# Performance work log

Hardware: AMD Instinct MI355X
Metric: run time of the kernel (lower is better)

## Reference

```python
import jax, jax.numpy as jnp
import numpy as np

# Instant-NGP style multi-resolution hash grid encoding
L = 16          # n_levels
F = 2           # n_feat_per_entry
D = 3           # spatial dim
T = 2 ** 19     # hashmap entries per level
B = 2 ** 20     # number of query points
BASE_RES, MAX_RES = 16, 512
PRIMES = (1, 2654435761, 805459861)  # NGP spatial hash primes


def setup_inputs() -> dict:
    key = jax.random.key(0)
    k1, k2 = jax.random.split(key)
    xyz = jax.random.uniform(k1, (B, D), dtype=jnp.float32)  # points in [0,1)^3
    offsets = np.arange(L + 1, dtype=np.int32) * T            # len L+1, offsets[-1] = n_total_embed
    n_total = int(offsets[-1])
    embeddings = (jax.random.uniform(k2, (n_total, F), dtype=jnp.float32) * 2.0 - 1.0) * 1e-4
    growth = np.exp(np.log(MAX_RES / BASE_RES) / (L - 1))
    resolutions = np.floor(BASE_RES * growth ** np.arange(L)).astype(np.int32)  # len L
    return {
        "xyz": xyz,
        "embeddings": embeddings,
        "offsets": jnp.asarray(offsets),
        "resolutions": jnp.asarray(resolutions),
        "min_xyz": jnp.zeros((D,), jnp.float32),
        "max_xyz": jnp.ones((D,), jnp.float32),
    }


def _encode(xyz, embeddings, offsets, resolutions, min_xyz, max_xyz):
    Bn, Dn = xyz.shape
    n_grid = 2 ** Dn  # corners of a cell
    # normalize to [0,1]; points outside the box are zeroed (valid mask)
    u = (xyz - min_xyz) / (max_xyz - min_xyz)                      # (B,D)
    valid = jnp.all((u >= 0.0) & (u <= 1.0), axis=-1)              # (B,)
    res = resolutions.astype(xyz.dtype)                            # (L,)
    pos = u[:, None, :] * res[None, :, None]                       # (B,L,D)
    pos0 = jnp.clip(jnp.floor(pos), 0.0, res[None, :, None] - 1.0) # lower cell corner
    frac = pos - pos0                                              # (B,L,D) in [0,1]
    # all 2^D corner offsets, bit d of corner c
    bits = jnp.asarray([[(c >> d) & 1 for d in range(Dn)] for c in range(n_grid)])  # (2^D, D)
    corners = pos0[:, :, None, :].astype(jnp.uint32) + bits[None, None].astype(jnp.uint32)  # (B,L,2^D,D)
    # trilinear weights: prod_d (frac if bit else 1-frac)
    fb = frac[:, :, None, :]
    w = jnp.prod(jnp.where(bits[None, None].astype(bool), fb, 1.0 - fb), axis=-1)  # (B,L,2^D)
    # spatial hash: xor of coord_d * prime_d (uint32 wraparound), mod level table size
    primes = jnp.asarray(PRIMES[:Dn], dtype=jnp.uint32)
    hp = corners * primes                                          # (B,L,2^D,D) uint32
    h = hp[..., 0]
    for d in range(1, Dn):
        h = h ^ hp[..., d]
    sizes = (offsets[1:] - offsets[:-1]).astype(jnp.uint32)        # (L,)
    idx = (h % sizes[None, :, None]).astype(jnp.int32) + offsets[:-1][None, :, None]  # (B,L,2^D)
    gathered = embeddings[idx]                                     # (B,L,2^D,F)
    out = jnp.einsum("blc,blcf->blf", w, gathered)                 # (B,L,F)
    out = out * valid[:, None, None].astype(out.dtype)
    return out.reshape(Bn, -1)                                     # (B, L*F)


def reference(xyz, embeddings, offsets, resolutions, min_xyz, max_xyz):
    return _encode(xyz, embeddings, offsets, resolutions, min_xyz, max_xyz)
```

## Files before the change

### kernel.cpp

```cpp
#include <hip/hip_runtime.h>

#define NLVL 16
#define NDENSE 7
#define BDENSE_CAP 600000

typedef float f32x2 __attribute__((ext_vector_type(2)));
typedef float f32x4 __attribute__((ext_vector_type(4)));
typedef _Float16 f16x2 __attribute__((ext_vector_type(2)));
typedef unsigned u32x2 __attribute__((ext_vector_type(2)));

__device__ __forceinline__ unsigned hash3(unsigned x, unsigned y, unsigned z) {
    return x ^ (y * 2654435761u) ^ (z * 805459861u);
}

__device__ __forceinline__ unsigned bdense_total(const int* __restrict__ resolutions,
                                                 unsigned bdoff[NDENSE]) {
    unsigned acc = 0;
    for (int ll = 0; ll < NDENSE; ++ll) {
        unsigned R = (unsigned)resolutions[ll];
        bdoff[ll] = acc;
        acc += R * R * (R + 1u);
    }
    return acc;
}

__global__ __launch_bounds__(256) void convert_fp16_kernel(
    const float* __restrict__ emb,
    _Float16*    __restrict__ htab,
    int n_entries)
{
    int i = blockIdx.x * 256 + (int)threadIdx.x;
    if (i >= n_entries) return;
    f32x2 v = reinterpret_cast<const f32x2*>(emb)[i];
    f16x2 h;
    h.x = (_Float16)v.x;
    h.y = (_Float16)v.y;
    reinterpret_cast<f16x2*>(htab)[i] = h;
}

__global__ __launch_bounds__(256) void bdensify_kernel(
    const unsigned* __restrict__ htab32,
    const int*      __restrict__ offsets,
    const int*      __restrict__ resolutions,
    unsigned*       __restrict__ bdense)
{
    unsigned bdoff[NDENSE];
    unsigned total = bdense_total(resolutions, bdoff);
    if (total > BDENSE_CAP) total = BDENSE_CAP;
    unsigned tid = blockIdx.x * 256u + threadIdx.x;
    if (tid >= total) return;
    int l = 0;
    while (l < NDENSE - 1 && tid >= bdoff[l + 1]) ++l;
    unsigned idx = tid - bdoff[l];
    unsigned R = (unsigned)resolutions[l];
    unsigned cx = idx % R;
    unsigned t  = idx / R;
    unsigned cy = t % R;
    unsigned z  = t / R;
    unsigned off  = (unsigned)offsets[l];
    unsigned size = (unsigned)offsets[l + 1] - off;
    unsigned mask = size - 1u;
    bool pow2 = (size & mask) == 0u;
    const unsigned* src = htab32 + off;

    unsigned q[4];
    {
        unsigned h = hash3(cx,      cy,      z);
        q[0] = src[pow2 ? (h & mask) : (h % size)];
    }
    {
        unsigned h = hash3(cx + 1u, cy,      z);
        q[1] = src[pow2 ? (h & mask) : (h % size)];
    }
    {
        unsigned h = hash3(cx,      cy + 1u, z);
        q[2] = src[pow2 ? (h & mask) : (h % size)];
    }
    {
        unsigned h = hash3(cx + 1u, cy + 1u, z);
        q[3] = src[pow2 ? (h & mask) : (h % size)];
    }
    __builtin_memcpy(bdense + (size_t)tid * 4u, q, 16);
}

__global__ __launch_bounds__(256) void encode_kernel(
    const float* __restrict__ xyz,
    const float* __restrict__ emb,
    const _Float16* __restrict__ htab,
    const int*   __restrict__ offsets,
    const int*   __restrict__ resolutions,
    const float* __restrict__ min_xyz,
    const float* __restrict__ max_xyz,
    const unsigned* __restrict__ bdense,
    float*       __restrict__ scratch,
    float*       __restrict__ out,
    int B, int use_bdense, int use_scratch, int use_fp16)
{
    const int g = blockIdx.x & 15;
    const int chunk = blockIdx.x >> 4;
    const int l = (g < 8) ? (8 + g) : (((g - 8) + (chunk >> 6)) & 7);
    const int p = chunk * 256 + (int)threadIdx.x;
    if (p >= B) return;

    const float res = (float)resolutions[l];
    const unsigned off  = (unsigned)offsets[l];
    const unsigned size = (unsigned)offsets[l + 1] - off;
    const unsigned mask = size - 1u;
    const bool pow2 = (size & mask) == 0u;
    const float mn0 = min_xyz[0], mn1 = min_xyz[1], mn2 = min_xyz[2];
    const float mx0 = max_xyz[0], mx1 = max_xyz[1], mx2 = max_xyz[2];

    const float x = xyz[p * 3 + 0];
    const float y = xyz[p * 3 + 1];
    const float z = xyz[p * 3 + 2];
    const float ux = (x - mn0) / (mx0 - mn0);
    const float uy = (y - mn1) / (mx1 - mn1);
    const float uz = (z - mn2) / (mx2 - mn2);
    const bool valid = (ux >= 0.0f) & (ux <= 1.0f) &
                       (uy >= 0.0f) & (uy <= 1.0f) &
                       (uz >= 0.0f) & (uz <= 1.0f);

    const float rm1 = res - 1.0f;
    const float px = ux * res, py = uy * res, pz = uz * res;
    const float p0x = fminf(fmaxf(floorf(px), 0.0f), rm1);
    const float p0y = fminf(fmaxf(floorf(py), 0.0f), rm1);
    const float p0z = fminf(fmaxf(floorf(pz), 0.0f), rm1);
    const float fx = px - p0x, fy = py - p0y, fz = pz - p0z;
    const float gx = 1.0f - fx, gy = 1.0f - fy, gz = 1.0f - fz;
    const unsigned cx0 = (unsigned)p0x;
    const unsigned cy0 = (unsigned)p0y;
    const unsigned cz0 = (unsigned)p0z;

    const unsigned P1 = 2654435761u;
    const unsigned P2 = 805459861u;

    float o0 = 0.0f, o1 = 0.0f;

    bool bdense_ok = false;
    unsigned bdoff[NDENSE];
    if (use_bdense && l < NDENSE) {
        unsigned total = bdense_total(resolutions, bdoff);
        bdense_ok = (total <= BDENSE_CAP);
    }

    if (bdense_ok) {
        const unsigned R = (unsigned)resolutions[l];
        const unsigned base = bdoff[l] + (cz0 * R + cy0) * R + cx0;
        unsigned q0[4], q1[4];
        __builtin_memcpy(q0, bdense + (size_t)base * 4u, 16);
        __builtin_memcpy(q1, bdense + (size_t)(base + R * R) * 4u, 16);
        f16x2 e0 = __builtin_bit_cast(f16x2, q0[0]);
        f16x2 e1 = __builtin_bit_cast(f16x2, q0[1]);
        f16x2 e2 = __builtin_bit_cast(f16x2, q0[2]);
        f16x2 e3 = __builtin_bit_cast(f16x2, q0[3]);
        f16x2 e4 = __builtin_bit_cast(f16x2, q1[0]);
        f16x2 e5 = __builtin_bit_cast(f16x2, q1[1]);
        f16x2 e6 = __builtin_bit_cast(f16x2, q1[2]);
        f16x2 e7 = __builtin_bit_cast(f16x2, q1[3]);
        o0 += (gx * gy * gz) * (float)e0.x;  o1 += (gx * gy * gz) * (float)e0.y;
        o0 += (fx * gy * gz) * (float)e1.x;  o1 += (fx * gy * gz) * (float)e1.y;
        o0 += (gx * fy * gz) * (float)e2.x;  o1 += (gx * fy * gz) * (float)e2.y;
        o0 += (fx * fy * gz) * (float)e3.x;  o1 += (fx * fy * gz) * (float)e3.y;
        o0 += (gx * gy * fz) * (float)e4.x;  o1 += (gx * gy * fz) * (float)e4.y;
        o0 += (fx * gy * fz) * (float)e5.x;  o1 += (fx * gy * fz) * (float)e5.y;
        o0 += (gx * fy * fz) * (float)e6.x;  o1 += (gx * fy * fz) * (float)e6.y;
        o0 += (fx * fy * fz) * (float)e7.x;  o1 += (fx * fy * fz) * (float)e7.y;
    } else if (use_fp16 && pow2) {
        const unsigned* lvl32 = reinterpret_cast<const unsigned*>(htab) + off;
        const u32x2*    lvlp  = reinterpret_cast<const u32x2*>(lvl32);
        unsigned m4[4], h0a[4];
        u32x2 pr[4];
#pragma unroll
        for (int pi = 0; pi < 4; ++pi) {
            unsigned by = (unsigned)(pi & 1);
            unsigned bz = (unsigned)(pi >> 1);
            unsigned m = ((cy0 + by) * P1) ^ ((cz0 + bz) * P2);
            unsigned h0 = (cx0 ^ m) & mask;
            m4[pi] = m; h0a[pi] = h0;
            pr[pi] = lvlp[h0 >> 1];
        }
        unsigned e0b[4], e1b[4];
        if ((cx0 & 1u) == 0u) {
#pragma unroll
            for (int pi = 0; pi < 4; ++pi) {
                bool hi = (h0a[pi] & 1u) != 0u;
                e0b[pi] = hi ? pr[pi].y : pr[pi].x;
                e1b[pi] = hi ? pr[pi].x : pr[pi].y;
            }
        } else {
#pragma unroll
            for (int pi = 0; pi < 4; ++pi) {
                unsigned h1 = ((cx0 + 1u) ^ m4[pi]) & mask;
                e1b[pi] = lvl32[h1];
                e0b[pi] = (h0a[pi] & 1u) ? pr[pi].y : pr[pi].x;
            }
        }
#pragma unroll
        for (int pi = 0; pi < 4; ++pi) {
            unsigned by = (unsigned)(pi & 1);
            unsigned bz = (unsigned)(pi >> 1);
            float wy = by ? fy : gy;
            float wz = bz ? fz : gz;
            float wyz = wy * wz;
            f16x2 e0 = __builtin_bit_cast(f16x2, e0b[pi]);
            f16x2 e1 = __builtin_bit_cast(f16x2, e1b[pi]);
            float w0 = gx * wyz;
            float w1 = fx * wyz;
            o0 += w0 * (float)e0.x;  o1 += w0 * (float)e0.y;
            o0 += w1 * (float)e1.x;  o1 += w1 * (float)e1.y;
        }
    } else {
        const f32x2* lvl = reinterpret_cast<const f32x2*>(emb) + off;
#pragma unroll
        for (int c = 0; c < 8; ++c) {
            unsigned bx = (unsigned)(c & 1);
            unsigned by = (unsigned)((c >> 1) & 1);
            unsigned bz = (unsigned)((c >> 2) & 1);
            unsigned h = hash3(cx0 + bx, cy0 + by, cz0 + bz);
            unsigned hm = pow2 ? (h & mask) : (h % size);
            f32x2 e = lvl[hm];
            float w = (bx ? fx : gx) * (by ? fy : gy);
            w = w * (bz ? fz : gz);
            o0 += w * e.x;
            o1 += w * e.y;
        }
    }

    if (!valid) { o0 = 0.0f; o1 = 0.0f; }
    if (use_scratch) {
        f16x2 h; h.x = (_Float16)o0; h.y = (_Float16)o1;
        unsigned hb = __builtin_bit_cast(unsigned, h);
        unsigned* op = reinterpret_cast<unsigned*>(scratch) + (size_t)l * B + p;
        __builtin_nontemporal_store(hb, op);
    } else {
        f32x2 r; r.x = o0; r.y = o1;
        f32x2* op = reinterpret_cast<f32x2*>(out + (size_t)p * (NLVL * 2) + l * 2);
        __builtin_nontemporal_store(r, op);
    }
}

__global__ __launch_bounds__(256) void transpose_kernel(
    const float* __restrict__ scratch,
    float*       __restrict__ out,
    int B)
{
    __shared__ float tile[64][33];
    const int p0 = blockIdx.x * 64;
    const int tid = (int)threadIdx.x;

    const unsigned* src = reinterpret_cast<const unsigned*>(scratch);
#pragma unroll
    for (int k = 0; k < 4; ++k) {
        int it = tid + k * 256;
        int l  = it >> 6;
        int pi = it & 63;
        int p  = p0 + pi;
        unsigned vb = (p < B) ? src[(size_t)l * B + p] : 0u;
        f16x2 v = __builtin_bit_cast(f16x2, vb);
        tile[pi][2 * l]     = (float)v.x;
        tile[pi][2 * l + 1] = (float)v.y;
    }
    __syncthreads();

    const int pl = tid >> 2;
    const int q  = tid & 3;
    const int p  = p0 + pl;
    if (p >= B) return;
    float vals[8];
#pragma unroll
    for (int j = 0; j < 8; ++j) vals[j] = tile[pl][q * 8 + j];
    f32x4 lo, hi;
    lo.x = vals[0]; lo.y = vals[1]; lo.z = vals[2]; lo.w = vals[3];
    hi.x = vals[4]; hi.y = vals[5]; hi.z = vals[6]; hi.w = vals[7];
    f32x4* dst = reinterpret_cast<f32x4*>(out + (size_t)p * 32 + q * 8);
    __builtin_nontemporal_store(lo, dst);
    __builtin_nontemporal_store(hi, dst + 1);
}

extern "C" void kernel_launch(void* const* d_in, const int* in_sizes, int n_in,
                              void* d_out, int out_size, void* d_ws, size_t ws_size,
                              hipStream_t stream) {
    const float* xyz        = (const float*)d_in[0];
    const float* embeddings = (const float*)d_in[1];
    const int*   offsets    = (const int*)d_in[2];
    const int*   resolutions= (const int*)d_in[3];
    const float* min_xyz    = (const float*)d_in[4];
    const float* max_xyz    = (const float*)d_in[5];
    float* out = (float*)d_out;

    int B = in_sizes[0] / 3;
    int n_entries = in_sizes[1] / 2;

    size_t scratch_bytes = (size_t)B * NLVL * 4;
    size_t htab_bytes    = (size_t)n_entries * 4;
    size_t bdense_bytes  = (size_t)BDENSE_CAP * 16;

    int use_scratch = (ws_size >= scratch_bytes) ? 1 : 0;
    size_t htab_off = use_scratch ? scratch_bytes : 0;
    int use_fp16 = (ws_size >= htab_off + htab_bytes) ? 1 : 0;
    size_t bdense_off = htab_off + (use_fp16 ? htab_bytes : 0);
    int use_bdense = (use_fp16 && ws_size >= bdense_off + bdense_bytes) ? 1 : 0;

    float*    scratch = (float*)d_ws;
    _Float16* htab    = (_Float16*)((char*)d_ws + htab_off);
    unsigned* bdense  = (unsigned*)((char*)d_ws + bdense_off);

    if (use_fp16) {
        int cgrid = (n_entries + 255) / 256;
        convert_fp16_kernel<<<cgrid, 256, 0, stream>>>(embeddings, htab, n_entries);
    }
    if (use_bdense) {
        int pgrid = (BDENSE_CAP + 255) / 256;
        bdensify_kernel<<<pgrid, 256, 0, stream>>>(
            (const unsigned*)htab, offsets, resolutions, bdense);
    }
    int nchunks = (B + 255) / 256;
    int grid = nchunks * NLVL;
    encode_kernel<<<grid, 256, 0, stream>>>(
        xyz, embeddings, htab, offsets, resolutions, min_xyz, max_xyz,
        bdense, scratch, out, B, use_bdense, use_scratch, use_fp16);
    if (use_scratch) {
        int tgrid = (B + 63) / 64;
        transpose_kernel<<<tgrid, 256, 0, stream>>>(scratch, out, B);
    }
}
```

Before: 417.1 us.

## Process four points per thread with vectorized xyz loads and scratch stores

Each encode thread now handles four consecutive points. It loads their coordinates with three 16-byte loads, issues all gather loads for the four points before accumulating, and writes the fp16 scratch results as one 16-byte nontemporal store. The aim is more memory-level parallelism per thread and fewer, wider load and store instructions. In exchange, the grid is four times smaller, which lowers occupancy and wave count and raises register pressure. The chunk-based level interleave also changes, since chunk>>6 now spans four times as many points.

Result: faster. 401.3 us (-3.8%).

```diff
diff --git a/kernel.cpp b/kernel.cpp
--- a/kernel.cpp
+++ b/kernel.cpp
@@ -3,11 +3,13 @@
 #define NLVL 16
 #define NDENSE 7
 #define BDENSE_CAP 600000
+#define PPT 4
 
 typedef float f32x2 __attribute__((ext_vector_type(2)));
 typedef float f32x4 __attribute__((ext_vector_type(4)));
 typedef _Float16 f16x2 __attribute__((ext_vector_type(2)));
 typedef unsigned u32x2 __attribute__((ext_vector_type(2)));
+typedef unsigned u32x4 __attribute__((ext_vector_type(4)));
 
 __device__ __forceinline__ unsigned hash3(unsigned x, unsigned y, unsigned z) {
     return x ^ (y * 2654435761u) ^ (z * 805459861u);
@@ -99,8 +101,8 @@
     const int g = blockIdx.x & 15;
     const int chunk = blockIdx.x >> 4;
     const int l = (g < 8) ? (8 + g) : (((g - 8) + (chunk >> 6)) & 7);
-    const int p = chunk * 256 + (int)threadIdx.x;
-    if (p >= B) return;
+    const int p0 = chunk * (256 * PPT) + (int)threadIdx.x * PPT;
+    if (p0 >= B) return;
 
     const float res = (float)resolutions[l];
     const unsigned off  = (unsigned)offsets[l];
@@ -110,31 +112,51 @@
     const float mn0 = min_xyz[0], mn1 = min_xyz[1], mn2 = min_xyz[2];
     const float mx0 = max_xyz[0], mx1 = max_xyz[1], mx2 = max_xyz[2];
 
-    const float x = xyz[p * 3 + 0];
-    const float y = xyz[p * 3 + 1];
-    const float z = xyz[p * 3 + 2];
-    const float ux = (x - mn0) / (mx0 - mn0);
-    const float uy = (y - mn1) / (mx1 - mn1);
-    const float uz = (z - mn2) / (mx2 - mn2);
-    const bool valid = (ux >= 0.0f) & (ux <= 1.0f) &
-                       (uy >= 0.0f) & (uy <= 1.0f) &
-                       (uz >= 0.0f) & (uz <= 1.0f);
-
-    const float rm1 = res - 1.0f;
-    const float px = ux * res, py = uy * res, pz = uz * res;
-    const float p0x = fminf(fmaxf(floorf(px), 0.0f), rm1);
-    const float p0y = fminf(fmaxf(floorf(py), 0.0f), rm1);
-    const float p0z = fminf(fmaxf(floorf(pz), 0.0f), rm1);
-    const float fx = px - p0x, fy = py - p0y, fz = pz - p0z;
-    const float gx = 1.0f - fx, gy = 1.0f - fy, gz = 1.0f - fz;
-    const unsigned cx0 = (unsigned)p0x;
-    const unsigned cy0 = (unsigned)p0y;
-    const unsigned cz0 = (unsigned)p0z;
-
     const unsigned P1 = 2654435761u;
     const unsigned P2 = 805459861u;
 
-    float o0 = 0.0f, o1 = 0.0f;
+    float X[PPT], Y[PPT], Z[PPT];
+    if (p0 + PPT <= B) {
+        f32x4 v0, v1, v2;
+        __builtin_memcpy(&v0, xyz + (size_t)p0 * 3,      16);
+        __builtin_memcpy(&v1, xyz + (size_t)p0 * 3 + 4,  16);
+        __builtin_memcpy(&v2, xyz + (size_t)p0 * 3 + 8,  16);
+        X[0] = v0.x; Y[0] = v0.y; Z[0] = v0.z;
+        X[1] = v0.w; Y[1] = v1.x; Z[1] = v1.y;
+        X[2] = v1.z; Y[2] = v1.w; Z[2] = v2.x;
+        X[3] = v2.y; Y[3] = v2.z; Z[3] = v2.w;
+    } else {
+#pragma unroll
+        for (int i = 0; i < PPT; ++i) {
+            int p = p0 + i; if (p > B - 1) p = B - 1;
+            X[i] = xyz[p * 3 + 0]; Y[i] = xyz[p * 3 + 1]; Z[i] = xyz[p * 3 + 2];
+        }
+    }
+
+    float fxa[PPT], fya[PPT], fza[PPT], qxa[PPT], qya[PPT], qza[PPT];
+    unsigned cxa[PPT], cya[PPT], cza[PPT];
+    bool valid[PPT];
+#pragma unroll
+    for (int i = 0; i < PPT; ++i) {
+        float ux = (X[i] - mn0) / (mx0 - mn0);
+        float uy = (Y[i] - mn1) / (mx1 - mn1);
+        float uz = (Z[i] - mn2) / (mx2 - mn2);
+        valid[i] = (ux >= 0.0f) & (ux <= 1.0f) &
+                   (uy >= 0.0f) & (uy <= 1.0f) &
+                   (uz >= 0.0f) & (uz <= 1.0f);
+        float rm1 = res - 1.0f;
+        float px = ux * res, py = uy * res, pz = uz * res;
+        float p0x = fminf(fmaxf(floorf(px), 0.0f), rm1);
+        float p0y = fminf(fmaxf(floorf(py), 0.0f), rm1);
+        float p0z = fminf(fmaxf(floorf(pz), 0.0f), rm1);
+        fxa[i] = px - p0x; fya[i] = py - p0y; fza[i] = pz - p0z;
+        qxa[i] = 1.0f - fxa[i]; qya[i] = 1.0f - fya[i]; qza[i] = 1.0f - fza[i];
+        cxa[i] = (unsigned)p0x; cya[i] = (unsigned)p0y; cza[i] = (unsigned)p0z;
+    }
+
+    float o0a[PPT], o1a[PPT];
+#pragma unroll
+    for (int i = 0; i < PPT; ++i) { o0a[i] = 0.0f; o1a[i] = 0.0f; }
 
     bool bdense_ok = false;
     unsigned bdoff[NDENSE];
@@ -145,97 +167,159 @@
 
     if (bdense_ok) {
         const unsigned R = (unsigned)resolutions[l];
-        const unsigned base = bdoff[l] + (cz0 * R + cy0) * R + cx0;
-        unsigned q0[4], q1[4];
-        __builtin_memcpy(q0, bdense + (size_t)base * 4u, 16);
-        __builtin_memcpy(q1, bdense + (size_t)(base + R * R) * 4u, 16);
-        f16x2 e0 = __builtin_bit_cast(f16x2, q0[0]);
-        f16x2 e1 = __builtin_bit_cast(f16x2, q0[1]);
-        f16x2 e2 = __builtin_bit_cast(f16x2, q0[2]);
-        f16x2 e3 = __builtin_bit_cast(f16x2, q0[3]);
-        f16x2 e4 = __builtin_bit_cast(f16x2, q1[0]);
-        f16x2 e5 = __builtin_bit_cast(f16x2, q1[1]);
-        f16x2 e6 = __builtin_bit_cast(f16x2, q1[2]);
-        f16x2 e7 = __builtin_bit_cast(f16x2, q1[3]);
-        o0 += (gx * gy * gz) * (float)e0.x;  o1 += (gx * gy * gz) * (float)e0.y;
-        o0 += (fx * gy * gz) * (float)e1.x;  o1 += (fx * gy * gz) * (float)e1.y;
-        o0 += (gx * fy * gz) * (float)e2.x;  o1 += (gx * fy * gz) * (float)e2.y;
-        o0 += (fx * fy * gz) * (float)e3.x;  o1 += (fx * fy * gz) * (float)e3.y;
-        o0 += (gx * gy * fz) * (float)e4.x;  o1 += (gx * gy * fz) * (float)e4.y;
-        o0 += (fx * gy * fz) * (float)e5.x;  o1 += (fx * gy * fz) * (float)e5.y;
-        o0 += (gx * fy * fz) * (float)e6.x;  o1 += (gx * fy * fz) * (float)e6.y;
-        o0 += (fx * fy * fz) * (float)e7.x;  o1 += (fx * fy * fz) * (float)e7.y;
+        unsigned base[PPT];
+#pragma unroll
+        for (int i = 0; i < PPT; ++i)
+            base[i] = bdoff[l] + (cza[i] * R + cya[i]) * R + cxa[i];
+        unsigned q0[PPT][4], q1[PPT][4];
+#pragma unroll
+        for (int i = 0; i < PPT; ++i)
+            __builtin_memcpy(q0[i], bdense + (size_t)base[i] * 4u, 16);
+#pragma unroll
+        for (int i = 0; i < PPT; ++i)
+            __builtin_memcpy(q1[i], bdense + (size_t)(base[i] + R * R) * 4u, 16);
+#pragma unroll
+        for (int i = 0; i < PPT; ++i) {
+            float fx = fxa[i], fy = fya[i], fz = fza[i];
+            float gx = qxa[i], gy = qya[i], gz = qza[i];
+            f16x2 e0 = __builtin_bit_cast(f16x2, q0[i][0]);
+            f16x2 e1 = __builtin_bit_cast(f16x2, q0[i][1]);
+            f16x2 e2 = __builtin_bit_cast(f16x2, q0[i][2]);
+            f16x2 e3 = __builtin_bit_cast(f16x2, q0[i][3]);
+            f16x2 e4 = __builtin_bit_cast(f16x2, q1[i][0]);
+            f16x2 e5 = __builtin_bit_cast(f16x2, q1[i][1]);
+            f16x2 e6 = __builtin_bit_cast(f16x2, q1[i][2]);
+            f16x2 e7 = __builtin_bit_cast(f16x2, q1[i][3]);
+            float o0 = 0.0f, o1 = 0.0f;
+            o0 += (gx * gy * gz) * (float)e0.x;  o1 += (gx * gy * gz) * (float)e0.y;
+            o0 += (fx * gy * gz) * (float)e1.x;  o1 += (fx * gy * gz) * (float)e1.y;
+            o0 += (gx * fy * gz) * (float)e2.x;  o1 += (gx * fy * gz) * (float)e2.y;
+            o0 += (fx * fy * gz) * (float)e3.x;  o1 += (fx * fy * gz) * (float)e3.y;
+            o0 += (gx * gy * fz) * (float)e4.x;  o1 += (gx * gy * fz) * (float)e4.y;
+            o0 += (fx * gy * fz) * (float)e5.x;  o1 += (fx * gy * fz) * (float)e5.y;
+            o0 += (gx * fy * fz) * (float)e6.x;  o1 += (gx * fy * fz) * (float)e6.y;
+            o0 += (fx * fy * fz) * (float)e7.x;  o1 += (fx * fy * fz) * (float)e7.y;
+            o0a[i] = o0; o1a[i] = o1;
+        }
     } else if (use_fp16 && pow2) {
         const unsigned* lvl32 = reinterpret_cast<const unsigned*>(htab) + off;
         const u32x2*    lvlp  = reinterpret_cast<const u32x2*>(lvl32);
-        unsigned m4[4], h0a[4];
-        u32x2 pr[4];
-#pragma unroll
-        for (int pi = 0; pi < 4; ++pi) {
-            unsigned by = (unsigned)(pi & 1);
-            unsigned bz = (unsigned)(pi >> 1);
-            unsigned m = ((cy0 + by) * P1) ^ ((cz0 + bz) * P2);
-            unsigned h0 = (cx0 ^ m) & mask;
-            m4[pi] = m; h0a[pi] = h0;
-            pr[pi] = lvlp[h0 >> 1];
-        }
-        unsigned e0b[4], e1b[4];
-        if ((cx0 & 1u) == 0u) {
+        u32x2 pr[PPT][4];
+#pragma unroll
+        for (int i = 0; i < PPT; ++i) {
 #pragma unroll
             for (int pi = 0; pi < 4; ++pi) {
-                bool hi = (h0a[pi] & 1u) != 0u;
-                e0b[pi] = hi ? pr[pi].y : pr[pi].x;
-                e1b[pi] = hi ? pr[pi].x : pr[pi].y;
+                unsigned m = ((cya[i] + (unsigned)(pi & 1)) * P1) ^
+                             ((cza[i] + (unsigned)(pi >> 1)) * P2);
+                unsigned h0 = (cxa[i] ^ m) & mask;
+                pr[i][pi] = lvlp[h0 >> 1];
             }
-        } else {
+        }
+#pragma unroll
+        for (int i = 0; i < PPT; ++i) {
+            float fx = fxa[i], fy = fya[i], fz = fza[i];
+            float gx = qxa[i], gy = qya[i], gz = qza[i];
+            bool odd = (cxa[i] & 1u) != 0u;
+            float o0 = 0.0f, o1 = 0.0f;
 #pragma unroll
             for (int pi = 0; pi < 4; ++pi) {
-                unsigned h1 = ((cx0 + 1u) ^ m4[pi]) & mask;
-                e1b[pi] = lvl32[h1];
-                e0b[pi] = (h0a[pi] & 1u) ? pr[pi].y : pr[pi].x;
+                unsigned m = ((cya[i] + (unsigned)(pi & 1)) * P1) ^
+                             ((cza[i] + (unsigned)(pi >> 1)) * P2);
+                unsigned h0 = (cxa[i] ^ m) & mask;
+                bool hi = (h0 & 1u) != 0u;
+                unsigned e0b = hi ? pr[i][pi].y : pr[i][pi].x;
+                unsigned e1b;
+                if (odd) {
+                    unsigned h1 = ((cxa[i] + 1u) ^ m) & mask;
+                    e1b = lvl32[h1];
+                } else {
+                    e1b = hi ? pr[i][pi].x : pr[i][pi].y;
+                }
+                float wy = (pi & 1) ? fy : gy;
+                float wz = (pi >> 1) ? fz : gz;
+                float wyz = wy * wz;
+                f16x2 e0 = __builtin_bit_cast(f16x2, e0b);
+                f16x2 e1 = __builtin_bit_cast(f16x2, e1b);
+                float w0 = gx * wyz;
+                float w1 = fx * wyz;
+                o0 += w0 * (float)e0.x;  o1 += w0 * (float)e0.y;
+                o0 += w1 * (float)e1.x;  o1 += w1 * (float)e1.y;
             }
-        }
-#pragma unroll
-        for (int pi = 0; pi < 4; ++pi) {
-            unsigned by = (unsigned)(pi & 1);
-            unsigned bz = (unsigned)(pi >> 1);
-            float wy = by ? fy : gy;
-            float wz = bz ? fz : gz;
-            float wyz = wy * wz;
-            f16x2 e0 = __builtin_bit_cast(f16x2, e0b[pi]);
-            f16x2 e1 = __builtin_bit_cast(f16x2, e1b[pi]);
-            float w0 = gx * wyz;
-            float w1 = fx * wyz;
-            o0 += w0 * (float)e0.x;  o1 += w0 * (float)e0.y;
-            o0 += w1 * (float)e1.x;  o1 += w1 * (float)e1.y;
+            o0a[i] = o0; o1a[i] = o1;
         }
     } else {
         const f32x2* lvl = reinterpret_cast<const f32x2*>(emb) + off;
 #pragma unroll
-        for (int c = 0; c < 8; ++c) {
-            unsigned bx = (unsigned)(c & 1);
-            unsigned by = (unsigned)((c >> 1) & 1);
-            unsigned bz = (unsigned)((c >> 2) & 1);
-            unsigned h = hash3(cx0 + bx, cy0 + by, cz0 + bz);
-            unsigned hm = pow2 ? (h & mask) : (h % size);
-            f32x2 e = lvl[hm];
-            float w = (bx ? fx : gx) * (by ? fy : gy);
-            w = w * (bz ? fz : gz);
-            o0 += w * e.x;
-            o1 += w * e.y;
-        }
-    }
-
-    if (!valid) { o0 = 0.0f; o1 = 0.0f; }
+        for (int i = 0; i < PPT; ++i) {
+            float fx = fxa[i], fy = fya[i], fz = fza[i];
+            float gx = qxa[i], gy = qya[i], gz = qza[i];
+            float o0 = 0.0f, o1 = 0.0f;
+#pragma unroll
+            for (int c = 0; c < 8; ++c) {
+                unsigned bx = (unsigned)(c & 1);
+                unsigned by = (unsigned)((c >> 1) & 1);
+                unsigned bz = (unsigned)((c >> 2) & 1);
+                unsigned h = hash3(cxa[i] + bx, cya[i] + by, cza[i] + bz);
+                unsigned hm = pow2 ? (h & mask) : (h % size);
+                f32x2 e = lvl[hm];
+                float w = (bx ? fx : gx) * (by ? fy : gy);
+                w = w * (bz ? fz : gz);
+                o0 += w * e.x;
+                o1 += w * e.y;
+            }
+            o0a[i] = o0; o1a[i] = o1;
+        }
+    }
+
+#pragma unroll
+    for (int i = 0; i < PPT; ++i) {
+        if (!valid[i]) { o0a[i] = 0.0f; o1a[i] = 0.0f; }
+    }
+
     if (use_scratch) {
-        f16x2 h; h.x = (_Float16)o0; h.y = (_Float16)o1;
-        unsigned hb = __builtin_bit_cast(unsigned, h);
-        unsigned* op = reinterpret_cast<unsigned*>(scratch) + (size_t)l * B + p;
-        __builtin_nontemporal_store(hb, op);
+        unsigned hb0, hb1, hb2, hb3;
+        {
+            f16x2 h; h.x = (_Float16)o0a[0]; h.y = (_Float16)o1a[0];
+            hb0 = __builtin_bit_cast(unsigned, h);
+        }
+        {
+            f16x2 h; h.x = (_Float16)o0a[1]; h.y = (_Float16)o1a[1];
+            hb1 = __builtin_bit_cast(unsigned, h);
+        }
+        {
+            f16x2 h; h.x = (_Float16)o0a[2]; h.y = (_Float16)o1a[2];
+            hb2 = __builtin_bit_cast(unsigned, h);
+        }
+        {
+            f16x2 h; h.x = (_Float16)o0a[3]; h.y = (_Float16)o1a[3];
+            hb3 = __builtin_bit_cast(unsigned, h);
+        }
+        if (p0 + PPT <= B) {
+            u32x4 sv; sv.x = hb0; sv.y = hb1; sv.z = hb2; sv.w = hb3;
+            u32x4* op = reinterpret_cast<u32x4*>(
+                reinterpret_cast<unsigned*>(scratch) + (size_t)l * B + p0);
+            __builtin_nontemporal_store(sv, op);
+        } else {
+            unsigned hbs[PPT] = {hb0, hb1, hb2, hb3};
+#pragma unroll
+            for (int i = 0; i < PPT; ++i) {
+                int p = p0 + i;
+                if (p < B) {
+                    unsigned* op = reinterpret_cast<unsigned*>(scratch) + (size_t)l * B + p;
+                    __builtin_nontemporal_store(hbs[i], op);
+                }
+            }
+        }
     } else {
-        f32x2 r; r.x = o0; r.y = o1;
-        f32x2* op = reinterpret_cast<f32x2*>(out + (size_t)p * (NLVL * 2) + l * 2);
-        __builtin_nontemporal_store(r, op);
+#pragma unroll
+        for (int i = 0; i < PPT; ++i) {
+            int p = p0 + i;
+            if (p < B) {
+                f32x2 r; r.x = o0a[i]; r.y = o1a[i];
+                f32x2* op = reinterpret_cast<f32x2*>(out + (size_t)p * (NLVL * 2) + l * 2);
+                __builtin_nontemporal_store(r, op);
+            }
+        }
     }
 }
 
@@ -314,7 +398,7 @@
         bdensify_kernel<<<pgrid, 256, 0, stream>>>(
             (const unsigned*)htab, offsets, resolutions, bdense);
     }
-    int nchunks = (B + 255) / 256;
+    int nchunks = (B + (256 * PPT) - 1) / (256 * PPT);
     int grid = nchunks * NLVL;
     encode_kernel<<<grid, 256, 0, stream>>>(
         xyz, embeddings, htab, offsets, resolutions, min_xyz, max_xyz,
```
